# Kernel tuning notes

Measured on AMD Instinct MI355X. Metric: run time of the kernel, lower is better.

## Reference

```python
import jax, jax.numpy as jnp
import numpy as np

B, H, W, C = 4, 64, 64, 512
G = 32  # GroupNorm groups
EPS = 1e-6


def setup_inputs() -> dict:
    key = jax.random.key(0)
    ks = jax.random.split(key, 9)
    s = C ** -0.5
    return {
        "x": jax.random.normal(ks[0], (B, H, W, C), dtype=jnp.float32),
        "gn_scale": jnp.ones((C,), dtype=jnp.float32),
        "gn_bias": jnp.zeros((C,), dtype=jnp.float32),
        "wq": jax.random.normal(ks[1], (C, C), dtype=jnp.float32) * s,
        "bq": jnp.zeros((C,), dtype=jnp.float32),
        "wk": jax.random.normal(ks[2], (C, C), dtype=jnp.float32) * s,
        "bk": jnp.zeros((C,), dtype=jnp.float32),
        "wv": jax.random.normal(ks[3], (C, C), dtype=jnp.float32) * s,
        "bv": jnp.zeros((C,), dtype=jnp.float32),
        "wo": jax.random.normal(ks[4], (C, C), dtype=jnp.float32) * s,
        "bo": jnp.zeros((C,), dtype=jnp.float32),
    }


def reference(x, gn_scale, gn_bias, wq, bq, wk, bk, wv, bv, wo, bo):
    b, h, w, c = x.shape
    # GroupNorm(32, eps=1e-6): normalize over (H, W, channels-within-group)
    xg = x.reshape(b, h, w, G, c // G)
    mean = xg.mean(axis=(1, 2, 4), keepdims=True)
    var = xg.var(axis=(1, 2, 4), keepdims=True)
    hn = ((xg - mean) * jax.lax.rsqrt(var + EPS)).reshape(b, h, w, c)
    hn = hn * gn_scale + gn_bias
    # 1x1 convs == per-pixel matmuls
    n = h * w
    hf = hn.reshape(b, n, c)
    q = hf @ wq + bq  # [b, n, c]
    k = hf @ wk + bk
    v = hf @ wv + bv
    # attention with materialized scores (faithful to source math)
    scores = jnp.einsum('bqc,bkc->bqk', q, k) * (c ** -0.5)
    attn = jax.nn.softmax(scores, axis=2)
    o = jnp.einsum('bkc,bqk->bqc', v, attn)  # [b, n, c]
    o = o @ wo + bo
    return o.reshape(b, h, w, c) + x
```

## Files before the change

kernel.cpp:

```cpp
#include <hip/hip_runtime.h>
#include <stdint.h>

typedef unsigned short u16;
typedef long i64;
typedef __bf16 bf16x8 __attribute__((ext_vector_type(8)));
typedef float f32x4 __attribute__((ext_vector_type(4)));
typedef uint32_t u32x2 __attribute__((ext_vector_type(2)));
typedef uint32_t u32x4 __attribute__((ext_vector_type(4)));

#define NB 4
#define NC 512
#define NG 32
#define NSEQ 4096
#define NM (NB*NSEQ)

#define MFMA_(a,b,c) __builtin_amdgcn_mfma_f32_16x16x32_bf16(a,b,c,0,0,0)
#define MFMA8_(a,b,c) __builtin_amdgcn_mfma_f32_16x16x32_fp8_fp8(a,b,c,0,0,0)

__device__ __forceinline__ u16 f2bf(float f){
  uint32_t u = __builtin_bit_cast(uint32_t, f);
  u += 0x7FFFu + ((u >> 16) & 1u);
  return (u16)(u >> 16);
}
__device__ __forceinline__ float bfu(uint32_t lo16){
  return __builtin_bit_cast(float, lo16 << 16);
}
__device__ __forceinline__ uint32_t pk2(float a, float b){
  return (uint32_t)f2bf(a) | ((uint32_t)f2bf(b) << 16);
}

__device__ __forceinline__ void gll16(const void* g, void* l){
  __builtin_amdgcn_global_load_lds(
      (const __attribute__((address_space(1))) void*)g,
      (__attribute__((address_space(3))) void*)l, 16, 0, 0);
}

__global__ void k_zero(float* p, int n){
  int i = blockIdx.x*blockDim.x + threadIdx.x;
  if (i < n) p[i] = 0.f;
}

__global__ __launch_bounds__(256) void k_gn_stats2(const float* __restrict__ x,
    u16* __restrict__ xbf, float* __restrict__ stats){
  int blk = blockIdx.x;
  int b = blk >> 6, ch = blk & 63;
  int t = threadIdx.x;
  int colv = t & 127;
  int r0 = ch*64 + (t >> 7);
  const float* xp = x  + (size_t)b*NSEQ*NC + (size_t)r0*NC + colv*4;
  u16* xb       = xbf + (size_t)b*NSEQ*NC + (size_t)r0*NC + colv*4;
  float s1 = 0.f, s2 = 0.f;
  #pragma unroll 4
  for (int i = 0; i < 32; i++){
    float4 v = *(const float4*)(xp + (size_t)i*2*NC);
    s1 += v.x+v.y+v.z+v.w;
    s2 += v.x*v.x+v.y*v.y+v.z*v.z+v.w*v.w;
    ushort4 o; o.x=f2bf(v.x); o.y=f2bf(v.y); o.z=f2bf(v.z); o.w=f2bf(v.w);
    *(ushort4*)(xb + (size_t)i*2*NC) = o;
  }
  s1 += __shfl_xor(s1,1); s2 += __shfl_xor(s2,1);
  s1 += __shfl_xor(s1,2); s2 += __shfl_xor(s2,2);
  __shared__ float ls1[4][16], ls2[4][16];
  int w = t >> 6, l = t & 63;
  if ((l & 3) == 0){ ls1[w][l>>2] = s1; ls2[w][l>>2] = s2; }
  __syncthreads();
  if (t < 32){
    int g = t;
    int wlo = g >> 4;
    float a1 = ls1[wlo][g&15] + ls1[wlo+2][g&15];
    float a2 = ls2[wlo][g&15] + ls2[wlo+2][g&15];
    atomicAdd(&stats[(b*NG+g)*2+0], a1);
    atomicAdd(&stats[(b*NG+g)*2+1], a2);
  }
}

__global__ __launch_bounds__(256) void k_gn_apply2(const u16* __restrict__ xbf,
    const float* __restrict__ stats, const float* __restrict__ gsc,
    const float* __restrict__ gbi, u16* __restrict__ hn){
  const float inv_cnt = 1.f/((float)NSEQ*16.f);
  size_t i = ((size_t)blockIdx.x*256 + threadIdx.x)*8;
  int c = (int)(i & 511);
  int b = (int)(i >> 21);
  int g = c >> 4;
  float s1 = stats[(b*NG+g)*2], s2 = stats[(b*NG+g)*2+1];
  float mean = s1*inv_cnt;
  float rstd = rsqrtf(s2*inv_cnt - mean*mean + 1e-6f);
  u32x4 v = *(const u32x4*)(xbf + i);
  float4 scA = *(const float4*)(gsc + c), scB = *(const float4*)(gsc + c + 4);
  float4 biA = *(const float4*)(gbi + c), biB = *(const float4*)(gbi + c + 4);
  const float sc[8] = {scA.x,scA.y,scA.z,scA.w,scB.x,scB.y,scB.z,scB.w};
  const float bi[8] = {biA.x,biA.y,biA.z,biA.w,biB.x,biB.y,biB.z,biB.w};
  u32x4 o;
  #pragma unroll
  for (int j = 0; j < 4; j++){
    float lo = bfu(v[j] & 0xFFFFu);
    float hi = __builtin_bit_cast(float, v[j] & 0xFFFF0000u);
    o[j] = pk2((lo-mean)*rstd*sc[2*j] + bi[2*j], (hi-mean)*rstd*sc[2*j+1] + bi[2*j+1]);
  }
  *(u32x4*)(hn + i) = o;
}

__global__ __launch_bounds__(256) void k_wtrans4(const float* __restrict__ wq, const float* __restrict__ wk,
    const float* __restrict__ wv, const float* __restrict__ wo,
    u16* __restrict__ wqkvT, u16* __restrict__ woT){
  int j = blockIdx.x*256 + threadIdx.x;
  int wsel = j >> 18, r = j & 262143;
  int n = r >> 9, k = r & 511;
  const float* src = wsel==0?wq : wsel==1?wk : wsel==2?wv : wo;
  u16 v = f2bf(src[k*512 + n]);
  if (wsel < 3) wqkvT[(size_t)wsel*262144 + r] = v;
  else          woT[r] = v;
}

__global__ __launch_bounds__(256) void k_sumred(const float* __restrict__ part, float* __restrict__ sums){
  int row = blockIdx.x*4 + (threadIdx.x >> 6);
  int l = threadIdx.x & 63;
  float s = part[(size_t)row*64 + l];
  #pragma unroll
  for (int o = 32; o; o >>= 1) s += __shfl_xor(s, o);
  if (l == 0) sums[row] = s;
}

__global__ __launch_bounds__(256) void k_pvred(const u16* __restrict__ op, const float* __restrict__ sums,
    u16* __restrict__ o){
  size_t i = ((size_t)blockIdx.x*256 + threadIdx.x)*8;
  int row = (int)(i >> 9);
  float inv = 1.f/sums[row];
  u32x4 a = __builtin_nontemporal_load((const u32x4*)(op + i));
  u32x4 b = __builtin_nontemporal_load((const u32x4*)(op + (size_t)NM*NC + i));
  uint32_t r[4];
  #pragma unroll
  for (int j=0;j<4;j++){
    float lo = (bfu(a[j] & 0xFFFFu) + bfu(b[j] & 0xFFFFu)) * inv;
    float hi = (__builtin_bit_cast(float, a[j] & 0xFFFF0000u) +
                __builtin_bit_cast(float, b[j] & 0xFFFF0000u)) * inv;
    r[j] = (uint32_t)f2bf(lo) | ((uint32_t)f2bf(hi) << 16);
  }
  *(uint4*)(o + i) = make_uint4(r[0], r[1], r[2], r[3]);
}

#define NTQ 16

__device__ __forceinline__ int dec_rl(int L, int p){ return 2*L + ((p>>2) ^ ((L>>1)&1)); }
__device__ __forceinline__ int dec_kq(int L, int p){
  int P01 = ((((L)&1)^((L>>2)&1))<<1) | (((L>>1)&1)^((L>>3)&1));
  return (p&3) ^ P01;
}
__device__ __forceinline__ int swz_off(int rl, int kq){
  int Pq = (((rl&1)^((rl>>2)&1))<<2) | ((((rl>>1)&1)^((rl>>3)&1))<<1) | (((rl>>2)&1)^((rl>>4)&1));
  return ((rl>>1)<<7) + ((Pq ^ kq)<<4);
}

__global__ __launch_bounds__(512, 4) void k_qkv(
    const u16* __restrict__ A, const u16* __restrict__ B,
    uint8_t* __restrict__ q8, uint8_t* __restrict__ k8, uint8_t* __restrict__ v8T,
    const float* __restrict__ bias0, const float* __restrict__ bias1, const float* __restrict__ bias2)
{
  __shared__ u16 LDS[36864];
  char* Lb = (char*)LDS;
  const int t = threadIdx.x;
  const int l = t & 63, w = t >> 6;
  const int wr = w >> 2, wc = w & 3;
  const int frow = l & 15, kq = l >> 4;
  const int nx = gridDim.x, ny = gridDim.y;
  int f = (int)blockIdx.y*nx + (int)blockIdx.x;
  const int nwg = nx*ny;
  f = (f & 7)*(nwg >> 3) + (f >> 3);
  const int bx = f % nx; const int by = f / nx;
  const int brow = by*128, bcol = bx*256;

  const int pA = t & 7;
  const int LA = t >> 3;
  const int LB0 = t >> 3, LB1 = 64 + (t >> 3);
  const int rlA  = dec_rl(LA, pA),  kqA  = dec_kq(LA, pA);
  const int rlB0 = dec_rl(LB0, pA), kqB0 = dec_kq(LB0, pA);
  const int rlB1 = dec_rl(LB1, pA), kqB1 = dec_kq(LB1, pA);
  const u16* Ap  = A + (size_t)(brow + rlA )*NC + kqA*8;
  const u16* Bp0 = B + (size_t)(bcol + rlB0)*NC + kqB0*8;
  const u16* Bp1 = B + (size_t)(bcol + rlB1)*NC + kqB1*8;

  auto stage = [&](int buf, int kt){
    const size_t ko = (size_t)kt*32;
    gll16(Bp0 + ko, Lb + buf*16384 + t*16);
    gll16(Bp1 + ko, Lb + buf*16384 + 8192 + t*16);
    gll16(Ap  + ko, Lb + 49152 + buf*8192 + t*16);
  };

  int offA[4], offB[4];
  #pragma unroll
  for (int m=0;m<4;m++) offA[m] = swz_off(wr*64 + m*16 + frow, kq);
  #pragma unroll
  for (int c=0;c<4;c++) offB[c] = swz_off(wc*64 + 4*frow + c, kq);

  f32x4 acc[4][4] = {};

  auto body = [&](int buf, int s){
    bf16x8 a4[4], b4[4];
    #pragma unroll
    for (int m=0;m<4;m++) a4[m] = *(const bf16x8*)(Lb + 49152 + buf*8192 + offA[m]);
    #pragma unroll
    for (int c=0;c<4;c++) b4[c] = *(const bf16x8*)(Lb + buf*16384 + offB[c]);
    const bool doStage = (s + 2 < NTQ);
    if (doStage){ int nb = buf+2; if (nb>=3) nb-=3; stage(nb, s+2); }
    asm volatile("s_waitcnt lgkmcnt(0)" ::: "memory");
    __builtin_amdgcn_sched_barrier(0);
    __builtin_amdgcn_s_setprio(1);
    #pragma unroll
    for (int m=0;m<4;m++)
      #pragma unroll
      for (int c=0;c<4;c++)
        acc[m][c] = MFMA_(a4[m], b4[c], acc[m][c]);
    __builtin_amdgcn_s_setprio(0);
    __builtin_amdgcn_sched_barrier(0);
    if (s + 1 < NTQ){
      if (doStage) asm volatile("s_waitcnt vmcnt(3)" ::: "memory");
      else         asm volatile("s_waitcnt vmcnt(0)" ::: "memory");
      __builtin_amdgcn_s_barrier();
    }
  };

  stage(0, 0); stage(1, 1);
  asm volatile("s_waitcnt vmcnt(3)" ::: "memory");
  __builtin_amdgcn_s_barrier();

  #pragma unroll
  for (int i = 0; i < 5; i++){
    body(0, i*3);
    body(1, i*3+1);
    body(2, i*3+2);
  }
  body(0, 15);

  const int col4 = wc*64 + 4*frow;
  const int seg = bcol >> 9;
  const int colr = (bcol & 511) + col4;
  if (seg < 2){
    uint8_t* dq = seg==0 ? q8 : k8;
    const float* bp = seg==0 ? bias0 : bias1;
    const float4 bi = *(const float4*)(bp + colr);
    #pragma unroll
    for (int m=0;m<4;m++){
      #pragma unroll
      for (int r=0;r<4;r++){
        const int rr = brow + wr*64 + m*16 + kq*4 + r;
        unsigned int pv = __builtin_amdgcn_cvt_pk_fp8_f32(acc[m][0][r]+bi.x, acc[m][1][r]+bi.y, 0u, false);
        pv = __builtin_amdgcn_cvt_pk_fp8_f32(acc[m][2][r]+bi.z, acc[m][3][r]+bi.w, pv, true);
        *(unsigned int*)&dq[(size_t)rr*NC + colr] = pv;
      }
    }
  } else {
    const float4 bi = *(const float4*)(bias2 + colr);
    const float bvs[4] = {bi.x, bi.y, bi.z, bi.w};
    #pragma unroll
    for (int m=0;m<4;m++){
      const int rr0 = brow + wr*64 + m*16 + kq*4;
      const int b = rr0 >> 12, sq = rr0 & 4095;
      #pragma unroll
      for (int n=0;n<4;n++){
        unsigned int pv = __builtin_amdgcn_cvt_pk_fp8_f32(acc[m][n][0]+bvs[n], acc[m][n][1]+bvs[n], 0u, false);
        pv = __builtin_amdgcn_cvt_pk_fp8_f32(acc[m][n][2]+bvs[n], acc[m][n][3]+bvs[n], pv, true);
        *(unsigned int*)&v8T[((size_t)(b*NC + colr + n) << 12) + sq] = pv;
      }
    }
  }
}

__device__ __forceinline__ int rdoff8(int rl, int ks){
  int slot8 = ((rl&1)<<3) | (((((ks>>1) ^ (rl>>1)) & 3))<<1) | (ks&1);
  return ((rl>>1)<<7) + (slot8<<3);
}
__device__ __forceinline__ int cmap64(int p){
  return (p & 192) + (((p & 15) << 2) | ((p >> 4) & 3));
}

__global__ __launch_bounds__(512, 4) void k_qk8(
    const uint8_t* __restrict__ Q8, const uint8_t* __restrict__ K8,
    uint8_t* __restrict__ P8, float* __restrict__ partsum, float alpha)
{
  __shared__ char LDS[73728];
  char* LA = LDS;
  char* LB = LDS + 24576;
  const int t = threadIdx.x;
  const int l = t & 63, w = t >> 6;
  const int wr = w >> 2, wc = w & 3;
  const int frow = l & 15, kq = l >> 4;
  int f = ((int)blockIdx.z*32 + (int)blockIdx.y)*16 + (int)blockIdx.x;
  f = (f & 7)*256 + (f >> 3);
  const int bx = f & 15; const int t2 = f >> 4;
  const int by = t2 & 31; const int bb = t2 >> 5;
  const int brow = by*128, bcol = bx*256;
  const size_t bOff = (size_t)bb*NSEQ*NC;

  const int Lp = t >> 3, p2 = t & 7;
  const int rlu = 2*Lp + (p2 >> 2);
  const int gru = (p2 & 3) ^ (Lp & 3);
  const uint8_t* Ap  = Q8 + bOff + (size_t)(brow + rlu)*NC + gru*16;
  const uint8_t* Bp0 = K8 + bOff + (size_t)(bcol + cmap64(rlu))*NC + gru*16;
  const uint8_t* Bp1 = K8 + bOff + (size_t)(bcol + cmap64(rlu + 128))*NC + gru*16;

  auto stage = [&](int buf, int kt){
    const size_t ko = (size_t)kt*64;
    gll16(Ap  + ko, LA + buf*8192 + t*16);
    gll16(Bp0 + ko, LB + buf*16384 + t*16);
    gll16(Bp1 + ko, LB + buf*16384 + 8192 + t*16);
  };

  int offA[4], offB[4];
  #pragma unroll
  for (int m=0;m<4;m++) offA[m] = rdoff8(wr*64 + m*16 + frow, kq);
  #pragma unroll
  for (int n=0;n<4;n++) offB[n] = rdoff8(wc*64 + n*16 + frow, kq);

  f32x4 acc[4][4] = {};

  auto body = [&](int buf, int s){
    i64 a0[4], a1[4], b0[4], b1[4];
    const char* Ab = LA + buf*8192;
    const char* Bb = LB + buf*16384;
    #pragma unroll
    for (int m=0;m<4;m++){ a0[m] = *(const i64*)(Ab + offA[m]); a1[m] = *(const i64*)(Ab + (offA[m]^32)); }
    #pragma unroll
    for (int n=0;n<4;n++){ b0[n] = *(const i64*)(Bb + offB[n]); b1[n] = *(const i64*)(Bb + (offB[n]^32)); }
    const bool doStage = (s + 2 < 8);
    if (doStage){ int nb = buf+2; if (nb>=3) nb-=3; stage(nb, s+2); }
    asm volatile("s_waitcnt lgkmcnt(0)" ::: "memory");
    __builtin_amdgcn_sched_barrier(0);
    __builtin_amdgcn_s_setprio(1);
    #pragma unroll
    for (int m=0;m<4;m++)
      #pragma unroll
      for (int n=0;n<4;n++){
        acc[m][n] = MFMA8_(a0[m], b0[n], acc[m][n]);
        acc[m][n] = MFMA8_(a1[m], b1[n], acc[m][n]);
      }
    __builtin_amdgcn_s_setprio(0);
    __builtin_amdgcn_sched_barrier(0);
    if (s + 1 < 8){
      if (doStage) asm volatile("s_waitcnt vmcnt(3)" ::: "memory");
      else         asm volatile("s_waitcnt vmcnt(0)" ::: "memory");
      __builtin_amdgcn_s_barrier();
    }
  };

  stage(0, 0); stage(1, 1);
  asm volatile("s_waitcnt vmcnt(3)" ::: "memory");
  __builtin_amdgcn_s_barrier();

  body(0,0); body(1,1); body(2,2); body(0,3);
  body(1,4); body(2,5); body(0,6); body(1,7);

  uint8_t* Pp = P8 + (size_t)bb*NSEQ*NSEQ;
  const int colp = bcol + wc*64 + 4*frow;
  #pragma unroll
  for (int m=0;m<4;m++){
    #pragma unroll
    for (int r=0;r<4;r++){
      const int rr = brow + wr*64 + m*16 + kq*4 + r;
      float e0 = __expf(alpha*acc[m][0][r]);
      float e1 = __expf(alpha*acc[m][1][r]);
      float e2 = __expf(alpha*acc[m][2][r]);
      float e3 = __expf(alpha*acc[m][3][r]);
      unsigned int p4 = __builtin_amdgcn_cvt_pk_fp8_f32(e0, e1, 0u, false);
      p4 = __builtin_amdgcn_cvt_pk_fp8_f32(e2, e3, p4, true);
      __builtin_nontemporal_store(p4, (unsigned int*)&Pp[(size_t)rr*NSEQ + colp]);
      float rs = e0 + e1 + e2 + e3;
      rs += __shfl_xor(rs, 1); rs += __shfl_xor(rs, 2);
      rs += __shfl_xor(rs, 4); rs += __shfl_xor(rs, 8);
      if (frow == 0)
        partsum[((size_t)bb*NSEQ + rr)*64 + bx*4 + wc] = rs;
    }
  }
}

__global__ __launch_bounds__(512, 4) void k_pv8(
    const uint8_t* __restrict__ P8, const uint8_t* __restrict__ V8,
    u16* __restrict__ opart)
{
  __shared__ char LDS[73728];
  char* LA = LDS;
  char* LB = LDS + 24576;
  const int t = threadIdx.x;
  const int l = t & 63, w = t >> 6;
  const int wr = w >> 2, wc = w & 3;
  const int frow = l & 15, kq = l >> 4;
  int f = ((int)blockIdx.z*32 + (int)blockIdx.y)*2 + (int)blockIdx.x;
  f = (f & 7)*64 + (f >> 3);
  const int bx = f & 1; const int t2 = f >> 1;
  const int by = t2 & 31; const int bz = t2 >> 5;
  const int bb = bz & 3; const int sp = bz >> 2;
  const int brow = by*128, bcol = bx*256;
  const int kOff = sp*(NSEQ/2);

  const int Lp = t >> 3, p2 = t & 7;
  const int rlu = 2*Lp + (p2 >> 2);
  const int gru = (p2 & 3) ^ (Lp & 3);
  const uint8_t* Ap  = P8 + (size_t)bb*NSEQ*NSEQ + (size_t)(brow + rlu)*NSEQ + kOff + gru*16;
  const uint8_t* Bp0 = V8 + (size_t)bb*NC*NSEQ + (size_t)(bcol + cmap64(rlu))*NSEQ + kOff + gru*16;
  const uint8_t* Bp1 = V8 + (size_t)bb*NC*NSEQ + (size_t)(bcol + cmap64(rlu + 128))*NSEQ + kOff + gru*16;

  auto stage = [&](int buf, int kt){
    const size_t ko = (size_t)kt*64;
    gll16(Ap  + ko, LA + buf*8192 + t*16);
    gll16(Bp0 + ko, LB + buf*16384 + t*16);
    gll16(Bp1 + ko, LB + buf*16384 + 8192 + t*16);
  };

  int offA[4], offB[4];
  #pragma unroll
  for (int m=0;m<4;m++) offA[m] = rdoff8(wr*64 + m*16 + frow, kq);
  #pragma unroll
  for (int n=0;n<4;n++) offB[n] = rdoff8(wc*64 + n*16 + frow, kq);

  f32x4 acc[4][4] = {};

  auto body = [&](int buf, int s){
    i64 a0[4], a1[4], b0[4], b1[4];
    const char* Ab = LA + buf*8192;
    const char* Bb = LB + buf*16384;
    #pragma unroll
    for (int m=0;m<4;m++){ a0[m] = *(const i64*)(Ab + offA[m]); a1[m] = *(const i64*)(Ab + (offA[m]^32)); }
    #pragma unroll
    for (int n=0;n<4;n++){ b0[n] = *(const i64*)(Bb + offB[n]); b1[n] = *(const i64*)(Bb + (offB[n]^32)); }
    const bool doStage = (s + 2 < 32);
    if (doStage){ int nb = buf+2; if (nb>=3) nb-=3; stage(nb, s+2); }
    asm volatile("s_waitcnt lgkmcnt(0)" ::: "memory");
    __builtin_amdgcn_sched_barrier(0);
    __builtin_amdgcn_s_setprio(1);
    #pragma unroll
    for (int m=0;m<4;m++)
      #pragma unroll
      for (int n=0;n<4;n++){
        acc[m][n] = MFMA8_(a0[m], b0[n], acc[m][n]);
        acc[m][n] = MFMA8_(a1[m], b1[n], acc[m][n]);
      }
    __builtin_amdgcn_s_setprio(0);
    __builtin_amdgcn_sched_barrier(0);
    if (s + 1 < 32){
      if (doStage) asm volatile("s_waitcnt vmcnt(3)" ::: "memory");
      else         asm volatile("s_waitcnt vmcnt(0)" ::: "memory");
      __builtin_amdgcn_s_barrier();
    }
  };

  stage(0, 0); stage(1, 1);
  asm volatile("s_waitcnt vmcnt(3)" ::: "memory");
  __builtin_amdgcn_s_barrier();

  #pragma unroll
  for (int i = 0; i < 10; i++){
    body(0, i*3);
    body(1, i*3+1);
    body(2, i*3+2);
  }
  body(0, 30); body(1, 31);

  u16* op = opart + (size_t)sp*NM*NC + (size_t)bb*NSEQ*NC;
  const int col4 = bcol + wc*64 + 4*frow;
  #pragma unroll
  for (int m=0;m<4;m++){
    #pragma unroll
    for (int r=0;r<4;r++){
      const int rr = brow + wr*64 + m*16 + kq*4 + r;
      u32x2 wv;
      wv[0] = pk2(acc[m][0][r], acc[m][1][r]);
      wv[1] = pk2(acc[m][2][r], acc[m][3][r]);
      __builtin_nontemporal_store(wv, (u32x2*)&op[(size_t)rr*NC + col4]);
    }
  }
}

__global__ __launch_bounds__(256, 3) void k_t256o(
    const u16* __restrict__ A, const u16* __restrict__ B,
    float* __restrict__ out, const float* __restrict__ bias, const float* __restrict__ res)
{
  __shared__ u16 LDS[24576];
  char* Lb = (char*)LDS;
  const int t = threadIdx.x;
  const int l = t & 63, w = t >> 6;
  const int wr = w >> 1, wc = w & 1;
  const int frow = l & 15, kq = l >> 4;
  int f = (int)blockIdx.y*4 + (int)blockIdx.x;
  f = (f & 7)*64 + (f >> 3);
  const int bx = f & 3; const int by = f >> 2;
  const int brow = by*128, bcol = bx*128;

  const int pA = t & 7;
  const int L0 = t >> 3;
  const int rl0 = dec_rl(L0, pA),      kq0 = dec_kq(L0, pA);
  const int rl1 = dec_rl(L0+32, pA),   kq1 = dec_kq(L0+32, pA);
  const u16* Ap0 = A + (size_t)(brow + rl0)*NC + kq0*8;
  const u16* Ap1 = A + (size_t)(brow + rl1)*NC + kq1*8;
  const u16* Bp0 = B + (size_t)(bcol + rl0)*NC + kq0*8;
  const u16* Bp1 = B + (size_t)(bcol + rl1)*NC + kq1*8;

  auto stage = [&](int buf, int kt){
    const size_t ko = (size_t)kt*32;
    gll16(Ap0 + ko, Lb + buf*16384 + t*16);
    gll16(Ap1 + ko, Lb + buf*16384 + 4096 + t*16);
    gll16(Bp0 + ko, Lb + buf*16384 + 8192 + t*16);
    gll16(Bp1 + ko, Lb + buf*16384 + 12288 + t*16);
  };

  int offA[4], offB[4];
  #pragma unroll
  for (int m=0;m<4;m++) offA[m] = swz_off(wr*64 + m*16 + frow, kq);
  #pragma unroll
  for (int c=0;c<4;c++) offB[c] = swz_off(wc*64 + 4*frow + c, kq);

  f32x4 acc[4][4] = {};

  auto body = [&](int buf, int s){
    bf16x8 a4[4], b4[4];
    #pragma unroll
    for (int m=0;m<4;m++) a4[m] = *(const bf16x8*)(Lb + buf*16384 + offA[m]);
    #pragma unroll
    for (int c=0;c<4;c++) b4[c] = *(const bf16x8*)(Lb + buf*16384 + 8192 + offB[c]);
    const bool doStage = (s + 2 < NTQ);
    if (doStage){ int nb = buf+2; if (nb>=3) nb-=3; stage(nb, s+2); }
    asm volatile("s_waitcnt lgkmcnt(0)" ::: "memory");
    __builtin_amdgcn_sched_barrier(0);
    __builtin_amdgcn_s_setprio(1);
    #pragma unroll
    for (int m=0;m<4;m++)
      #pragma unroll
      for (int c=0;c<4;c++)
        acc[m][c] = MFMA_(a4[m], b4[c], acc[m][c]);
    __builtin_amdgcn_s_setprio(0);
    __builtin_amdgcn_sched_barrier(0);
    if (s + 1 < NTQ){
      if (doStage) asm volatile("s_waitcnt vmcnt(4)" ::: "memory");
      else         asm volatile("s_waitcnt vmcnt(0)" ::: "memory");
      __builtin_amdgcn_s_barrier();
    }
  };

  stage(0, 0); stage(1, 1);
  asm volatile("s_waitcnt vmcnt(4)" ::: "memory");
  __builtin_amdgcn_s_barrier();

  #pragma unroll
  for (int i = 0; i < 5; i++){
    body(0, i*3);
    body(1, i*3+1);
    body(2, i*3+2);
  }
  body(0, 15);

  const int c = bcol + wc*64 + 4*frow;
  const float4 bi = *(const float4*)(bias + c);
  #pragma unroll
  for (int m=0;m<4;m++){
    #pragma unroll
    for (int r=0;r<4;r++){
      const int rr = brow + wr*64 + m*16 + kq*4 + r;
      const float4 rv = *(const float4*)(res + (size_t)rr*NC + c);
      float4 ov;
      ov.x = acc[m][0][r] + bi.x + rv.x;
      ov.y = acc[m][1][r] + bi.y + rv.y;
      ov.z = acc[m][2][r] + bi.z + rv.z;
      ov.w = acc[m][3][r] + bi.w + rv.w;
      *(float4*)&out[(size_t)rr*NC + c] = ov;
    }
  }
}

extern "C" void kernel_launch(void* const* d_in, const int* in_sizes, int n_in,
                              void* d_out, int out_size, void* d_ws, size_t ws_size,
                              hipStream_t stream){
  const float* x   = (const float*)d_in[0];
  const float* gsc = (const float*)d_in[1];
  const float* gbi = (const float*)d_in[2];
  const float* wq  = (const float*)d_in[3];
  const float* bq  = (const float*)d_in[4];
  const float* wk  = (const float*)d_in[5];
  const float* bk  = (const float*)d_in[6];
  const float* wv  = (const float*)d_in[7];
  const float* bv  = (const float*)d_in[8];
  const float* wo  = (const float*)d_in[9];
  const float* bo  = (const float*)d_in[10];
  float* out = (float*)d_out;

  char* wsp = (char*)d_ws;
  size_t off = 0;
  auto alloc = [&](size_t bytes)->void*{ void* p = wsp + off; off += (bytes + 255) & ~(size_t)255; return p; };
  float* stats   = (float*)alloc((size_t)NB*NG*2*sizeof(float));
  float* sums    = (float*)alloc((size_t)NM*sizeof(float));
  float* partsum = (float*)alloc((size_t)NM*64*sizeof(float));
  u16* xbf   = (u16*)alloc((size_t)NM*NC*2);
  u16* hn    = (u16*)alloc((size_t)NM*NC*2);
  u16* wqkvT = (u16*)alloc((size_t)3*NC*NC*2);
  u16* woT   = (u16*)alloc((size_t)NC*NC*2);
  uint8_t* q8 = (uint8_t*)alloc((size_t)NM*NC);
  uint8_t* k8 = (uint8_t*)alloc((size_t)NM*NC);
  uint8_t* v8 = (uint8_t*)alloc((size_t)NM*NC);
  u16* o     = (u16*)alloc((size_t)NM*NC*2);
  uint8_t* P8 = (uint8_t*)alloc((size_t)NB*NSEQ*NSEQ);
  u16* opart = xbf;

  k_zero<<<1,256,0,stream>>>(stats, NB*NG*2);
  k_gn_stats2<<<NB*64,256,0,stream>>>(x, xbf, stats);
  k_gn_apply2<<<4096,256,0,stream>>>(xbf, stats, gsc, gbi, hn);
  k_wtrans4<<<4096,256,0,stream>>>(wq, wk, wv, wo, wqkvT, woT);

  k_qkv<<<dim3(6,128,1),512,0,stream>>>(hn, wqkvT, q8, k8, v8, bq, bk, bv);

  const float scale = 0.044194173824159216f;
  k_qk8<<<dim3(16,32,NB),512,0,stream>>>(q8, k8, P8, partsum, scale);
  k_sumred<<<NM/4,256,0,stream>>>(partsum, sums);
  k_pv8<<<dim3(2,32,8),512,0,stream>>>(P8, v8, opart);
  k_pvred<<<NM*NC/8/256,256,0,stream>>>(opart, sums, o);
  k_t256o<<<dim3(4,128,1),256,0,stream>>>(o, woT, out, bo, x);
}
```

Baseline: 204.4 us.

## Switch QK^T fp8 kernel to 32x32x64 scaled MFMA with linear LDS layout

Replaces the 16x16x32 fp8 MFMA tiling in the QK scores kernel with the MI355X 32x32x64 f8f6f4 scaled MFMA (unit scales), so each wave issues four large MFMAs per k-step instead of thirty-two small ones. The swizzled LDS staging is replaced by a plain row-major layout read with 32-byte vector loads, and the epilogue is rewritten for the 32x32 accumulator layout. Risks include LDS bank conflicts from the unswizzled layout and a slower epilogue that now writes single bytes instead of packed 4-byte nontemporal stores.

```diff
diff --git a/kernel.cpp b/kernel.cpp
--- a/kernel.cpp
+++ b/kernel.cpp
@@ -5,6 +5,8 @@
 typedef long i64;
 typedef __bf16 bf16x8 __attribute__((ext_vector_type(8)));
 typedef float f32x4 __attribute__((ext_vector_type(4)));
+typedef float f32x16 __attribute__((ext_vector_type(16)));
+typedef int v8i __attribute__((ext_vector_type(8)));
 typedef uint32_t u32x2 __attribute__((ext_vector_type(2)));
 typedef uint32_t u32x4 __attribute__((ext_vector_type(4)));
 
@@ -16,6 +18,7 @@
 
 #define MFMA_(a,b,c) __builtin_amdgcn_mfma_f32_16x16x32_bf16(a,b,c,0,0,0)
 #define MFMA8_(a,b,c) __builtin_amdgcn_mfma_f32_16x16x32_fp8_fp8(a,b,c,0,0,0)
+#define MFMAX_(a,b,c) __builtin_amdgcn_mfma_scale_f32_32x32x64_f8f6f4(a,b,c,0,0,0,127,0,127)
 
 __device__ __forceinline__ u16 f2bf(float f){
   uint32_t u = __builtin_bit_cast(uint32_t, f);
@@ -283,7 +286,7 @@
   const int t = threadIdx.x;
   const int l = t & 63, w = t >> 6;
   const int wr = w >> 2, wc = w & 3;
-  const int frow = l & 15, kq = l >> 4;
+  const int l31 = l & 31, kh = l >> 5;
   int f = ((int)blockIdx.z*32 + (int)blockIdx.y)*16 + (int)blockIdx.x;
   f = (f & 7)*256 + (f >> 3);
   const int bx = f & 15; const int t2 = f >> 4;
@@ -291,12 +294,9 @@
   const int brow = by*128, bcol = bx*256;
   const size_t bOff = (size_t)bb*NSEQ*NC;
 
-  const int Lp = t >> 3, p2 = t & 7;
-  const int rlu = 2*Lp + (p2 >> 2);
-  const int gru = (p2 & 3) ^ (Lp & 3);
-  const uint8_t* Ap  = Q8 + bOff + (size_t)(brow + rlu)*NC + gru*16;
-  const uint8_t* Bp0 = K8 + bOff + (size_t)(bcol + cmap64(rlu))*NC + gru*16;
-  const uint8_t* Bp1 = K8 + bOff + (size_t)(bcol + cmap64(rlu + 128))*NC + gru*16;
+  const uint8_t* Ap  = Q8 + bOff + (size_t)(brow + (t>>2))*NC + (t&3)*16;
+  const uint8_t* Bp0 = K8 + bOff + (size_t)(bcol + (t>>2))*NC + (t&3)*16;
+  const uint8_t* Bp1 = K8 + bOff + (size_t)(bcol + 128 + (t>>2))*NC + (t&3)*16;
 
   auto stage = [&](int buf, int kt){
     const size_t ko = (size_t)kt*64;
@@ -305,34 +305,28 @@
     gll16(Bp1 + ko, LB + buf*16384 + 8192 + t*16);
   };
 
-  int offA[4], offB[4];
-  #pragma unroll
-  for (int m=0;m<4;m++) offA[m] = rdoff8(wr*64 + m*16 + frow, kq);
-  #pragma unroll
-  for (int n=0;n<4;n++) offB[n] = rdoff8(wc*64 + n*16 + frow, kq);
-
-  f32x4 acc[4][4] = {};
+  int offA[2], offB[2];
+  #pragma unroll
+  for (int mi=0;mi<2;mi++) offA[mi] = (wr*64 + mi*32 + l31)*64 + kh*32;
+  #pragma unroll
+  for (int ni=0;ni<2;ni++) offB[ni] = (wc*64 + ni*32 + l31)*64 + kh*32;
+
+  f32x16 acc[2][2] = {};
 
   auto body = [&](int buf, int s){
-    i64 a0[4], a1[4], b0[4], b1[4];
-    const char* Ab = LA + buf*8192;
-    const char* Bb = LB + buf*16384;
-    #pragma unroll
-    for (int m=0;m<4;m++){ a0[m] = *(const i64*)(Ab + offA[m]); a1[m] = *(const i64*)(Ab + (offA[m]^32)); }
-    #pragma unroll
-    for (int n=0;n<4;n++){ b0[n] = *(const i64*)(Bb + offB[n]); b1[n] = *(const i64*)(Bb + (offB[n]^32)); }
+    v8i a0 = *(const v8i*)(LA + buf*8192  + offA[0]);
+    v8i a1 = *(const v8i*)(LA + buf*8192  + offA[1]);
+    v8i b0 = *(const v8i*)(LB + buf*16384 + offB[0]);
+    v8i b1 = *(const v8i*)(LB + buf*16384 + offB[1]);
     const bool doStage = (s + 2 < 8);
     if (doStage){ int nb = buf+2; if (nb>=3) nb-=3; stage(nb, s+2); }
     asm volatile("s_waitcnt lgkmcnt(0)" ::: "memory");
     __builtin_amdgcn_sched_barrier(0);
     __builtin_amdgcn_s_setprio(1);
-    #pragma unroll
-    for (int m=0;m<4;m++)
-      #pragma unroll
-      for (int n=0;n<4;n++){
-        acc[m][n] = MFMA8_(a0[m], b0[n], acc[m][n]);
-        acc[m][n] = MFMA8_(a1[m], b1[n], acc[m][n]);
-      }
+    acc[0][0] = MFMAX_(a0, b0, acc[0][0]);
+    acc[0][1] = MFMAX_(a0, b1, acc[0][1]);
+    acc[1][0] = MFMAX_(a1, b0, acc[1][0]);
+    acc[1][1] = MFMAX_(a1, b1, acc[1][1]);
     __builtin_amdgcn_s_setprio(0);
     __builtin_amdgcn_sched_barrier(0);
     if (s + 1 < 8){
@@ -350,23 +344,23 @@
   body(1,4); body(2,5); body(0,6); body(1,7);
 
   uint8_t* Pp = P8 + (size_t)bb*NSEQ*NSEQ;
-  const int colp = bcol + wc*64 + 4*frow;
-  #pragma unroll
-  for (int m=0;m<4;m++){
-    #pragma unroll
-    for (int r=0;r<4;r++){
-      const int rr = brow + wr*64 + m*16 + kq*4 + r;
-      float e0 = __expf(alpha*acc[m][0][r]);
-      float e1 = __expf(alpha*acc[m][1][r]);
-      float e2 = __expf(alpha*acc[m][2][r]);
-      float e3 = __expf(alpha*acc[m][3][r]);
-      unsigned int p4 = __builtin_amdgcn_cvt_pk_fp8_f32(e0, e1, 0u, false);
-      p4 = __builtin_amdgcn_cvt_pk_fp8_f32(e2, e3, p4, true);
-      __builtin_nontemporal_store(p4, (unsigned int*)&Pp[(size_t)rr*NSEQ + colp]);
-      float rs = e0 + e1 + e2 + e3;
+  const int colg = bcol + wc*64 + l31;
+  #pragma unroll
+  for (int mi=0; mi<2; mi++){
+    #pragma unroll
+    for (int reg=0; reg<16; reg++){
+      const int rr = brow + wr*64 + mi*32 + (reg&3) + 8*(reg>>2) + 4*kh;
+      float e0 = __expf(alpha*acc[mi][0][reg]);
+      float e1 = __expf(alpha*acc[mi][1][reg]);
+      unsigned int c0 = __builtin_amdgcn_cvt_pk_fp8_f32(e0, e0, 0u, false);
+      unsigned int c1 = __builtin_amdgcn_cvt_pk_fp8_f32(e1, e1, 0u, false);
+      Pp[(size_t)rr*NSEQ + colg]      = (uint8_t)(c0 & 0xFF);
+      Pp[(size_t)rr*NSEQ + colg + 32] = (uint8_t)(c1 & 0xFF);
+      float rs = e0 + e1;
       rs += __shfl_xor(rs, 1); rs += __shfl_xor(rs, 2);
       rs += __shfl_xor(rs, 4); rs += __shfl_xor(rs, 8);
-      if (frow == 0)
+      rs += __shfl_xor(rs, 16);
+      if (l31 == 0)
         partsum[((size_t)bb*NSEQ + rr)*64 + bx*4 + wc] = rs;
     }
   }
```

Result: slower. 424.9 us (+107.8%).

## Drop split-K in PV kernel and fuse softmax normalization into its epilogue

Applied to the files above, without the earlier changes.

The PV matmul no longer splits the key dimension into two halves written to a temporary buffer and summed by a separate reduction kernel. Each block now covers the full 4096-long K loop with a 128x128 output tile (256 threads, 4 waves) and applies the 1/rowsum normalization directly before storing bf16 output. This removes one kernel launch and the round trip through a partial-output buffer. In exchange there is less parallelism per block, a longer serial K loop that is no longer unrolled, and a different tile shape for data reuse.

```diff
diff --git a/kernel.cpp b/kernel.cpp
--- a/kernel.cpp
+++ b/kernel.cpp
@@ -121,24 +121,6 @@
   if (l == 0) sums[row] = s;
 }
 
-__global__ __launch_bounds__(256) void k_pvred(const u16* __restrict__ op, const float* __restrict__ sums,
-    u16* __restrict__ o){
-  size_t i = ((size_t)blockIdx.x*256 + threadIdx.x)*8;
-  int row = (int)(i >> 9);
-  float inv = 1.f/sums[row];
-  u32x4 a = __builtin_nontemporal_load((const u32x4*)(op + i));
-  u32x4 b = __builtin_nontemporal_load((const u32x4*)(op + (size_t)NM*NC + i));
-  uint32_t r[4];
-  #pragma unroll
-  for (int j=0;j<4;j++){
-    float lo = (bfu(a[j] & 0xFFFFu) + bfu(b[j] & 0xFFFFu)) * inv;
-    float hi = (__builtin_bit_cast(float, a[j] & 0xFFFF0000u) +
-                __builtin_bit_cast(float, b[j] & 0xFFFF0000u)) * inv;
-    r[j] = (uint32_t)f2bf(lo) | ((uint32_t)f2bf(hi) << 16);
-  }
-  *(uint4*)(o + i) = make_uint4(r[0], r[1], r[2], r[3]);
-}
-
 #define NTQ 16
 
 __device__ __forceinline__ int dec_rl(int L, int p){ return 2*L + ((p>>2) ^ ((L>>1)&1)); }
@@ -372,37 +354,36 @@
   }
 }
 
-__global__ __launch_bounds__(512, 4) void k_pv8(
+__global__ __launch_bounds__(256, 3) void k_pv8f(
     const uint8_t* __restrict__ P8, const uint8_t* __restrict__ V8,
-    u16* __restrict__ opart)
+    const float* __restrict__ sums, u16* __restrict__ o)
 {
-  __shared__ char LDS[73728];
-  char* LA = LDS;
-  char* LB = LDS + 24576;
+  __shared__ char LDS[49152];
+  char* Lb = LDS;
   const int t = threadIdx.x;
   const int l = t & 63, w = t >> 6;
-  const int wr = w >> 2, wc = w & 3;
+  const int wr = w >> 1, wc = w & 1;
   const int frow = l & 15, kq = l >> 4;
-  int f = ((int)blockIdx.z*32 + (int)blockIdx.y)*2 + (int)blockIdx.x;
+  int f = ((int)blockIdx.z*32 + (int)blockIdx.y)*4 + (int)blockIdx.x;
   f = (f & 7)*64 + (f >> 3);
-  const int bx = f & 1; const int t2 = f >> 1;
-  const int by = t2 & 31; const int bz = t2 >> 5;
-  const int bb = bz & 3; const int sp = bz >> 2;
-  const int brow = by*128, bcol = bx*256;
-  const int kOff = sp*(NSEQ/2);
+  const int bx = f & 3; const int t2 = f >> 2;
+  const int by = t2 & 31; const int bb = t2 >> 5;
+  const int brow = by*128, bcol = bx*128;
 
   const int Lp = t >> 3, p2 = t & 7;
   const int rlu = 2*Lp + (p2 >> 2);
   const int gru = (p2 & 3) ^ (Lp & 3);
-  const uint8_t* Ap  = P8 + (size_t)bb*NSEQ*NSEQ + (size_t)(brow + rlu)*NSEQ + kOff + gru*16;
-  const uint8_t* Bp0 = V8 + (size_t)bb*NC*NSEQ + (size_t)(bcol + cmap64(rlu))*NSEQ + kOff + gru*16;
-  const uint8_t* Bp1 = V8 + (size_t)bb*NC*NSEQ + (size_t)(bcol + cmap64(rlu + 128))*NSEQ + kOff + gru*16;
+  const uint8_t* Ap0 = P8 + (size_t)bb*NSEQ*NSEQ + (size_t)(brow + rlu)*NSEQ + gru*16;
+  const uint8_t* Ap1 = P8 + (size_t)bb*NSEQ*NSEQ + (size_t)(brow + rlu + 64)*NSEQ + gru*16;
+  const uint8_t* Bp0 = V8 + (size_t)bb*NC*NSEQ + (size_t)(bcol + cmap64(rlu))*NSEQ + gru*16;
+  const uint8_t* Bp1 = V8 + (size_t)bb*NC*NSEQ + (size_t)(bcol + cmap64(rlu + 64))*NSEQ + gru*16;
 
   auto stage = [&](int buf, int kt){
     const size_t ko = (size_t)kt*64;
-    gll16(Ap  + ko, LA + buf*8192 + t*16);
-    gll16(Bp0 + ko, LB + buf*16384 + t*16);
-    gll16(Bp1 + ko, LB + buf*16384 + 8192 + t*16);
+    gll16(Ap0 + ko, Lb + buf*16384 + t*16);
+    gll16(Ap1 + ko, Lb + buf*16384 + 4096 + t*16);
+    gll16(Bp0 + ko, Lb + buf*16384 + 8192 + t*16);
+    gll16(Bp1 + ko, Lb + buf*16384 + 12288 + t*16);
   };
 
   int offA[4], offB[4];
@@ -415,13 +396,13 @@
 
   auto body = [&](int buf, int s){
     i64 a0[4], a1[4], b0[4], b1[4];
-    const char* Ab = LA + buf*8192;
-    const char* Bb = LB + buf*16384;
+    const char* Ab = Lb + buf*16384;
+    const char* Bb = Lb + buf*16384 + 8192;
     #pragma unroll
     for (int m=0;m<4;m++){ a0[m] = *(const i64*)(Ab + offA[m]); a1[m] = *(const i64*)(Ab + (offA[m]^32)); }
     #pragma unroll
     for (int n=0;n<4;n++){ b0[n] = *(const i64*)(Bb + offB[n]); b1[n] = *(const i64*)(Bb + (offB[n]^32)); }
-    const bool doStage = (s + 2 < 32);
+    const bool doStage = (s + 2 < 64);
     if (doStage){ int nb = buf+2; if (nb>=3) nb-=3; stage(nb, s+2); }
     asm volatile("s_waitcnt lgkmcnt(0)" ::: "memory");
     __builtin_amdgcn_sched_barrier(0);
@@ -435,35 +416,36 @@
       }
     __builtin_amdgcn_s_setprio(0);
     __builtin_amdgcn_sched_barrier(0);
-    if (s + 1 < 32){
-      if (doStage) asm volatile("s_waitcnt vmcnt(3)" ::: "memory");
+    if (s + 1 < 64){
+      if (doStage) asm volatile("s_waitcnt vmcnt(4)" ::: "memory");
       else         asm volatile("s_waitcnt vmcnt(0)" ::: "memory");
       __builtin_amdgcn_s_barrier();
     }
   };
 
   stage(0, 0); stage(1, 1);
-  asm volatile("s_waitcnt vmcnt(3)" ::: "memory");
+  asm volatile("s_waitcnt vmcnt(4)" ::: "memory");
   __builtin_amdgcn_s_barrier();
 
-  #pragma unroll
-  for (int i = 0; i < 10; i++){
+  #pragma unroll 1
+  for (int i = 0; i < 21; i++){
     body(0, i*3);
     body(1, i*3+1);
     body(2, i*3+2);
   }
-  body(0, 30); body(1, 31);
-
-  u16* op = opart + (size_t)sp*NM*NC + (size_t)bb*NSEQ*NC;
+  body(0, 63);
+
+  u16* op = o + (size_t)bb*NSEQ*NC;
   const int col4 = bcol + wc*64 + 4*frow;
   #pragma unroll
   for (int m=0;m<4;m++){
     #pragma unroll
     for (int r=0;r<4;r++){
       const int rr = brow + wr*64 + m*16 + kq*4 + r;
+      const float inv = 1.f/sums[(size_t)bb*NSEQ + rr];
       u32x2 wv;
-      wv[0] = pk2(acc[m][0][r], acc[m][1][r]);
-      wv[1] = pk2(acc[m][2][r], acc[m][3][r]);
+      wv[0] = pk2(acc[m][0][r]*inv, acc[m][1][r]*inv);
+      wv[1] = pk2(acc[m][2][r]*inv, acc[m][3][r]*inv);
       __builtin_nontemporal_store(wv, (u32x2*)&op[(size_t)rr*NC + col4]);
     }
   }
@@ -595,7 +577,6 @@
   uint8_t* v8 = (uint8_t*)alloc((size_t)NM*NC);
   u16* o     = (u16*)alloc((size_t)NM*NC*2);
   uint8_t* P8 = (uint8_t*)alloc((size_t)NB*NSEQ*NSEQ);
-  u16* opart = xbf;
 
   k_zero<<<1,256,0,stream>>>(stats, NB*NG*2);
   k_gn_stats2<<<NB*64,256,0,stream>>>(x, xbf, stats);
@@ -607,7 +588,6 @@
   const float scale = 0.044194173824159216f;
   k_qk8<<<dim3(16,32,NB),512,0,stream>>>(q8, k8, P8, partsum, scale);
   k_sumred<<<NM/4,256,0,stream>>>(partsum, sums);
-  k_pv8<<<dim3(2,32,8),512,0,stream>>>(P8, v8, opart);
-  k_pvred<<<NM*NC/8/256,256,0,stream>>>(opart, sums, o);
+  k_pv8f<<<dim3(4,32,NB),256,0,stream>>>(P8, v8, sums, o);
   k_t256o<<<dim3(4,128,1),256,0,stream>>>(o, woT, out, bo, x);
 }
```

After: 201.7 us. About the same (-1.3%).
